# Performance work log

Hardware: AMD Instinct MI355X
Metric: run time of the kernel (lower is better)

The kernel has to match this reference:

```python
import jax, jax.numpy as jnp
import numpy as np

HEADS = 8
DIM_HEAD = 64
SCALE = DIM_HEAD ** -0.5


def setup_inputs() -> dict:
    key = jax.random.key(0)
    k1, k2, k3 = jax.random.split(key, 3)
    b, n, dim = 2, 4096, 512
    inner = HEADS * DIM_HEAD
    x = jax.random.normal(k1, (b, n, dim), dtype=jnp.float32)
    w_qkv = jax.random.normal(k2, (dim, 3 * inner), dtype=jnp.float32) * (dim ** -0.5)
    w_out = jax.random.normal(k3, (inner, dim), dtype=jnp.float32) * (inner ** -0.5)
    b_out = jnp.zeros((dim,), dtype=jnp.float32)
    return {"x": x, "w_qkv": w_qkv, "w_out": w_out, "b_out": b_out}


def reference(x, w_qkv, w_out, b_out):
    b, n, dim = x.shape
    qkv = x @ w_qkv  # [b, n, 3*inner]
    q, k, v = jnp.split(qkv, 3, axis=-1)
    # b n (h d) -> b h n d
    split_heads = lambda t: t.reshape(b, n, HEADS, DIM_HEAD).transpose(0, 2, 1, 3)
    q, k, v = split_heads(q), split_heads(k), split_heads(v)
    dots = jnp.einsum('bhid,bhjd->bhij', q, k) * SCALE  # [b, h, n, n]
    attn = jax.nn.log_softmax(dots, axis=-1)  # NOTE: log-softmax, not softmax
    out = jnp.einsum('bhij,bhjd->bhid', attn, v)  # [b, h, n, d]
    out = out.transpose(0, 2, 1, 3).reshape(b, n, HEADS * DIM_HEAD)
    return out @ w_out + b_out + x
```

## Files before the change

kernel.cpp:

```cpp
#include <hip/hip_runtime.h>
#include <stdint.h>

#define NSEQ   4096
#define BATCH  2
#define NHEAD  8
#define DHEAD  64
#define DIM    512
#define NQKV   1536
#define MROWS  (BATCH*NSEQ)
#define NBH    (BATCH*NHEAD)

typedef float  f32x4 __attribute__((ext_vector_type(4)));
typedef short  s16x8 __attribute__((ext_vector_type(8)));

__device__ __forceinline__ unsigned short f2b(float f){
  unsigned int u = __float_as_uint(f);
  u += 0x7FFFu + ((u >> 16) & 1u);
  return (unsigned short)(u >> 16);
}
__device__ __forceinline__ float b2f(unsigned short h){
  return __uint_as_float(((unsigned int)h) << 16);
}
__device__ __forceinline__ void gld_lds16(const void* g, void* l){
  __builtin_amdgcn_global_load_lds((const __attribute__((address_space(1))) unsigned int*)g,
                                   (__attribute__((address_space(3))) unsigned int*)l, 16, 0, 0);
}

__global__ void k_cvt(const float* __restrict__ in, unsigned short* __restrict__ out, int n4){
  int i = blockIdx.x*blockDim.x + threadIdx.x;
  if (i < n4){
    float4 v = ((const float4*)in)[i];
    ushort4 o;
    o.x = f2b(v.x); o.y = f2b(v.y); o.z = f2b(v.z); o.w = f2b(v.w);
    ((ushort4*)out)[i] = o;
  }
}

__global__ void k_transpose(const float* __restrict__ in, unsigned short* __restrict__ out, int R, int C){
  __shared__ float t[32][33];
  const int cb = blockIdx.x*32, rb = blockIdx.y*32;
  const int tx = threadIdx.x & 31, ty = threadIdx.x >> 5;
  #pragma unroll
  for (int s = 0; s < 32; s += 8) t[ty+s][tx] = in[(size_t)(rb+ty+s)*C + cb + tx];
  __syncthreads();
  #pragma unroll
  for (int s = 0; s < 32; s += 8) out[(size_t)(cb+ty+s)*R + rb + tx] = f2b(t[tx][ty+s]);
}

__global__ __launch_bounds__(256) void k_qkv_gemm(
    const unsigned short* __restrict__ A,
    const unsigned short* __restrict__ Bt,
    unsigned short* __restrict__ qbuf, unsigned short* __restrict__ kbuf,
    unsigned short* __restrict__ vbuf){
  __shared__ __align__(16) unsigned short at[128*32];
  __shared__ __align__(16) unsigned short bt[128*32];
  const int n0 = blockIdx.x*128, m0 = blockIdx.y*128;
  const int tid = threadIdx.x, w = tid>>6, lane = tid&63;
  const int wr = (w>>1)*64, wc = (w&1)*64;
  f32x4 acc[4][4] = {};
  for (int ks = 0; ks < 16; ++ks){
    const int k0 = ks*32;
    #pragma unroll
    for (int i = 0; i < 2; ++i){
      const int slot = w*2 + i;
      const int r = slot*16 + (lane>>2);
      const int ch = (lane&3) ^ (r&3);
      gld_lds16(A  + (size_t)(m0+r)*DIM + k0 + ch*8, (char*)at + slot*1024);
      gld_lds16(Bt + (size_t)(n0+r)*DIM + k0 + ch*8, (char*)bt + slot*1024);
    }
    __syncthreads();
    s16x8 af[4], bfr[4];
    #pragma unroll
    for (int f = 0; f < 4; ++f){
      const int rr = wr + f*16 + (lane&15);
      af[f]  = *(const s16x8*)((const char*)at + rr*64 + ((((lane>>4)) ^ (rr&3))<<4));
      const int cc = wc + f*16 + (lane&15);
      bfr[f] = *(const s16x8*)((const char*)bt + cc*64 + ((((lane>>4)) ^ (cc&3))<<4));
    }
    #pragma unroll
    for (int fr = 0; fr < 4; ++fr)
      #pragma unroll
      for (int fc = 0; fc < 4; ++fc)
        acc[fr][fc] = __builtin_amdgcn_mfma_f32_16x16x32_bf16(af[fr], bfr[fc], acc[fr][fc], 0,0,0);
    __syncthreads();
  }
  const float QS = 0.18033688011112042f;
  #pragma unroll
  for (int fr = 0; fr < 4; ++fr){
    #pragma unroll
    for (int fc = 0; fc < 4; ++fc){
      const int col = n0 + wc + fc*16 + (lane&15);
      const int which = col >> 9;
      const int h = (col & 511) >> 6;
      const int d = col & 63;
      unsigned short* dst = (which==0) ? qbuf : ((which==1) ? kbuf : vbuf);
      #pragma unroll
      for (int r = 0; r < 4; ++r){
        const int row = m0 + wr + fr*16 + (lane>>4)*4 + r;
        const int b = row >> 12, n = row & 4095;
        float v = acc[fr][fc][r];
        if (which == 0) v *= QS;
        dst[(size_t)((b*NHEAD + h)*NSEQ + n)*DHEAD + d] = f2b(v);
      }
    }
  }
}

__global__ __launch_bounds__(256) void k_tpart(
    const unsigned short* __restrict__ kbuf, const unsigned short* __restrict__ vbuf,
    unsigned short* __restrict__ tpart, float* __restrict__ vsp){
  __shared__ __align__(16) unsigned short kt[64*64];
  __shared__ __align__(16) unsigned short vt[64*64];
  const int bh = blockIdx.y, jc = blockIdx.x;
  const unsigned short* K = kbuf + (size_t)bh*NSEQ*DHEAD;
  const unsigned short* V = vbuf + (size_t)bh*NSEQ*DHEAD;
  const int tid = threadIdx.x;
  const int d1 = (tid>>4)<<2, d2 = (tid&15)<<2;
  const int j0 = jc*64;
  #pragma unroll
  for (int c = 0; c < 2; ++c){
    const int q = tid + 256*c;
    const int row = q>>3, ch = q&7;
    *(float4*)((char*)kt + row*128 + ch*16) = *(const float4*)((const char*)K + (size_t)(j0+row)*128 + ch*16);
    *(float4*)((char*)vt + row*128 + ch*16) = *(const float4*)((const char*)V + (size_t)(j0+row)*128 + ch*16);
  }
  __syncthreads();
  float accT[4][4] = {{0.f}};
  float accV[4] = {0.f,0.f,0.f,0.f};
  for (int jj = 0; jj < 64; ++jj){
    const ushort4 k4 = *(const ushort4*)(kt + jj*64 + d1);
    const ushort4 v4 = *(const ushort4*)(vt + jj*64 + d2);
    float kf[4] = {b2f(k4.x), b2f(k4.y), b2f(k4.z), b2f(k4.w)};
    float vf[4] = {b2f(v4.x), b2f(v4.y), b2f(v4.z), b2f(v4.w)};
    #pragma unroll
    for (int a = 0; a < 4; ++a)
      #pragma unroll
      for (int b = 0; b < 4; ++b) accT[a][b] += kf[a]*vf[b];
    #pragma unroll
    for (int b = 0; b < 4; ++b) accV[b] += vf[b];
  }
  unsigned short* tp = tpart + ((size_t)bh*64 + jc)*4096;
  #pragma unroll
  for (int a = 0; a < 4; ++a)
    #pragma unroll
    for (int b = 0; b < 4; ++b) tp[(d1+a)*64 + (d2+b)] = f2b(accT[a][b]);
  if (tid < 16){
    #pragma unroll
    for (int b = 0; b < 4; ++b) vsp[((size_t)bh*64 + jc)*64 + d2 + b] = accV[b];
  }
}

__global__ void k_tred(const unsigned short* __restrict__ tpart, const float* __restrict__ vsp,
                       unsigned short* __restrict__ TB, float* __restrict__ vsum){
  const int blk = blockIdx.x;
  const int bh = blk >> 4, part = blk & 15;
  const int tid = threadIdx.x;
  const int idx = part*256 + tid;
  const int dd1 = idx>>6, dd2 = idx&63;
  float s = 0.f;
  #pragma unroll 8
  for (int pr = 0; pr < 64; ++pr) s += b2f(tpart[((size_t)bh*64 + pr)*4096 + idx]);
  TB[(size_t)bh*4096 + dd2*64 + dd1] = f2b(s);
  if (part == 0 && tid < 64){
    float v = 0.f;
    #pragma unroll 8
    for (int pr = 0; pr < 64; ++pr) v += vsp[((size_t)bh*64 + pr)*64 + tid];
    vsum[bh*64 + tid] = v;
  }
}

#define ASTAGE(U, BUFI) do { \
    const int ti_ = jbase + (((U)+phase)&15); \
    const size_t o_ = (size_t)ti_*64*DHEAD; \
    char* d_ = (char*)kt[BUFI]; \
    gld_lds16(kg0 + o_, d_ + s0*1024); \
    gld_lds16(kg1 + o_, d_ + s1*1024); } while(0)

#define ATILE(BUF) do { \
    const char* buf_ = (const char*)(BUF); \
    _Pragma("unroll") \
    for (int kk = 0; kk < 4; ++kk){ \
      const int r_ = kk*16 + (lane&15); \
      const s16x8 b0_ = *(const s16x8*)(buf_ + r_*128 + ((((lane>>4))   ^ (r_&7))<<4)); \
      const s16x8 b1_ = *(const s16x8*)(buf_ + r_*128 + (((4+(lane>>4)) ^ (r_&7))<<4)); \
      f32x4 a0_ = {0.f,0.f,0.f,0.f}, a1_ = {0.f,0.f,0.f,0.f}; \
      f32x4 a2_ = {0.f,0.f,0.f,0.f}, a3_ = {0.f,0.f,0.f,0.f}; \
      __builtin_amdgcn_s_setprio(1); \
      a0_ = __builtin_amdgcn_mfma_f32_16x16x32_bf16(aq[0][0], b0_, a0_, 0,0,0); \
      a0_ = __builtin_amdgcn_mfma_f32_16x16x32_bf16(aq[0][1], b1_, a0_, 0,0,0); \
      a1_ = __builtin_amdgcn_mfma_f32_16x16x32_bf16(aq[1][0], b0_, a1_, 0,0,0); \
      a1_ = __builtin_amdgcn_mfma_f32_16x16x32_bf16(aq[1][1], b1_, a1_, 0,0,0); \
      a2_ = __builtin_amdgcn_mfma_f32_16x16x32_bf16(aq[2][0], b0_, a2_, 0,0,0); \
      a2_ = __builtin_amdgcn_mfma_f32_16x16x32_bf16(aq[2][1], b1_, a2_, 0,0,0); \
      a3_ = __builtin_amdgcn_mfma_f32_16x16x32_bf16(aq[3][0], b0_, a3_, 0,0,0); \
      a3_ = __builtin_amdgcn_mfma_f32_16x16x32_bf16(aq[3][1], b1_, a3_, 0,0,0); \
      __builtin_amdgcn_s_setprio(0); \
      _Pragma("unroll") \
      for (int rr = 0; rr < 4; ++rr){ \
        lsum[0][rr] += __builtin_amdgcn_exp2f(a0_[rr]); \
        lsum[1][rr] += __builtin_amdgcn_exp2f(a1_[rr]); \
        lsum[2][rr] += __builtin_amdgcn_exp2f(a2_[rr]); \
        lsum[3][rr] += __builtin_amdgcn_exp2f(a3_[rr]); \
      } \
    } } while(0)

#define APHASE(U, LASTW) do { \
    if (LASTW) { asm volatile("s_waitcnt vmcnt(0)" ::: "memory"); } \
    else       { asm volatile("s_waitcnt vmcnt(2)" ::: "memory"); } \
    __builtin_amdgcn_s_barrier(); \
    asm volatile("" ::: "memory"); \
    if ((U) < 14) ASTAGE((U)+2, ((U)+2)&3); \
    ATILE(kt[(U)&3]); } while(0)

__global__ __launch_bounds__(256) void k_attn(
    const unsigned short* __restrict__ qbuf, const unsigned short* __restrict__ kbuf,
    float* __restrict__ ps){
  __shared__ __align__(16) unsigned short kt[4][64*64];
  const int bid = blockIdx.x;
  const int idx = bid >> 3;
  const int bh  = ((bid & 7) << 1) + (idx >> 6);
  const int rest = idx & 63;
  const int qchunk = rest >> 2;
  const int js = rest & 3;
  const int tid = threadIdx.x, w = tid>>6, lane = tid&63;
  const int q0 = qchunk*256 + w*64;
  const unsigned short* Q = qbuf + (size_t)bh*NSEQ*DHEAD;
  const unsigned short* K = kbuf + (size_t)bh*NSEQ*DHEAD;

  s16x8 aq[4][2];
  #pragma unroll
  for (int g = 0; g < 4; ++g){
    const int qrow = q0 + g*16 + (lane&15);
    aq[g][0] = *(const s16x8*)(Q + (size_t)qrow*DHEAD + ((lane>>4)<<3));
    aq[g][1] = *(const s16x8*)(Q + (size_t)qrow*DHEAD + 32 + ((lane>>4)<<3));
  }

  const int s0 = w*2, s1 = w*2 + 1;
  const int srow0 = s0*8 + (lane>>3), srow1 = s1*8 + (lane>>3);
  const int sch = ((lane&7) ^ (lane>>3));
  const unsigned short* kg0 = K + (size_t)srow0*DHEAD + sch*8;
  const unsigned short* kg1 = K + (size_t)srow1*DHEAD + sch*8;

  const int phase = (idx*5) & 15;
  const int jbase = js*16;

  ASTAGE(0, 0);
  ASTAGE(1, 1);

  float lsum[4][4] = {};
  APHASE(0,false);  APHASE(1,false);  APHASE(2,false);  APHASE(3,false);
  APHASE(4,false);  APHASE(5,false);  APHASE(6,false);  APHASE(7,false);
  APHASE(8,false);  APHASE(9,false);  APHASE(10,false); APHASE(11,false);
  APHASE(12,false); APHASE(13,false); APHASE(14,false); APHASE(15,true);

  #pragma unroll
  for (int m = 1; m < 16; m <<= 1)
    #pragma unroll
    for (int g = 0; g < 4; ++g)
      #pragma unroll
      for (int r = 0; r < 4; ++r) lsum[g][r] += __shfl_xor(lsum[g][r], m, 16);

  if ((lane&15) == 0){
    float* pp = ps + ((size_t)js*NBH + bh)*NSEQ;
    #pragma unroll
    for (int g = 0; g < 4; ++g)
      #pragma unroll
      for (int r = 0; r < 4; ++r)
        pp[q0 + g*16 + (lane>>4)*4 + r] = lsum[g][r];
  }
}

__global__ __launch_bounds__(256) void k_attn_fin(
    const unsigned short* __restrict__ qbuf, const unsigned short* __restrict__ TB,
    const float* __restrict__ vsum, const float* __restrict__ ps,
    unsigned short* __restrict__ om){
  const int bid = blockIdx.x;
  const int bh = bid >> 6, qchunk = bid & 63;
  const int tid = threadIdx.x, w = tid>>6, lane = tid&63;
  const int q0 = qchunk*64 + w*16;
  const unsigned short* Q = qbuf + (size_t)bh*NSEQ*DHEAD;
  const int qrow = q0 + (lane&15);
  const s16x8 aq0 = *(const s16x8*)(Q + (size_t)qrow*DHEAD + ((lane>>4)<<3));
  const s16x8 aq1 = *(const s16x8*)(Q + (size_t)qrow*DHEAD + 32 + ((lane>>4)<<3));
  const float* p0 = ps + (size_t)bh*NSEQ;
  const float* p1 = ps + ((size_t)NBH   + bh)*NSEQ;
  const float* p2 = ps + ((size_t)2*NBH + bh)*NSEQ;
  const float* p3 = ps + ((size_t)3*NBH + bh)*NSEQ;
  float lse2[4];
  #pragma unroll
  for (int r = 0; r < 4; ++r){
    const int n = q0 + (lane>>4)*4 + r;
    lse2[r] = log2f((p0[n] + p1[n]) + (p2[n] + p3[n]));
  }
  const unsigned short* tb = TB + (size_t)bh*4096;
  const int b = bh>>3, h = bh&7;
  #pragma unroll
  for (int fc = 0; fc < 4; ++fc){
    const int d2 = fc*16 + (lane&15);
    const s16x8 t0 = *(const s16x8*)(tb + d2*64 + ((lane>>4)<<3));
    const s16x8 t1 = *(const s16x8*)(tb + d2*64 + 32 + ((lane>>4)<<3));
    const float vs = vsum[bh*64 + d2];
    f32x4 acc = {0.f,0.f,0.f,0.f};
    acc = __builtin_amdgcn_mfma_f32_16x16x32_bf16(aq0, t0, acc, 0,0,0);
    acc = __builtin_amdgcn_mfma_f32_16x16x32_bf16(aq1, t1, acc, 0,0,0);
    #pragma unroll
    for (int r = 0; r < 4; ++r){
      const int n = q0 + (lane>>4)*4 + r;
      const float val = 0.6931471805599453f * (acc[r] - lse2[r]*vs);
      om[((size_t)b*NSEQ + n)*DIM + h*DHEAD + d2] = f2b(val);
    }
  }
}

__global__ __launch_bounds__(256) void k_out_gemm(
    const unsigned short* __restrict__ A,
    const unsigned short* __restrict__ Bt,
    const float* __restrict__ bias, const float* __restrict__ xres,
    float* __restrict__ out){
  __shared__ __align__(16) unsigned short at[128*32];
  __shared__ __align__(16) unsigned short bt[128*32];
  const int n0 = blockIdx.x*128, m0 = blockIdx.y*128;
  const int tid = threadIdx.x, w = tid>>6, lane = tid&63;
  const int wr = (w>>1)*64, wc = (w&1)*64;
  f32x4 acc[4][4] = {};
  for (int ks = 0; ks < 16; ++ks){
    const int k0 = ks*32;
    #pragma unroll
    for (int i = 0; i < 2; ++i){
      const int slot = w*2 + i;
      const int r = slot*16 + (lane>>2);
      const int ch = (lane&3) ^ (r&3);
      gld_lds16(A  + (size_t)(m0+r)*DIM + k0 + ch*8, (char*)at + slot*1024);
      gld_lds16(Bt + (size_t)(n0+r)*DIM + k0 + ch*8, (char*)bt + slot*1024);
    }
    __syncthreads();
    s16x8 af[4], bfr[4];
    #pragma unroll
    for (int f = 0; f < 4; ++f){
      const int rr = wr + f*16 + (lane&15);
      af[f]  = *(const s16x8*)((const char*)at + rr*64 + ((((lane>>4)) ^ (rr&3))<<4));
      const int cc = wc + f*16 + (lane&15);
      bfr[f] = *(const s16x8*)((const char*)bt + cc*64 + ((((lane>>4)) ^ (cc&3))<<4));
    }
    #pragma unroll
    for (int fr = 0; fr < 4; ++fr)
      #pragma unroll
      for (int fc = 0; fc < 4; ++fc)
        acc[fr][fc] = __builtin_amdgcn_mfma_f32_16x16x32_bf16(af[fr], bfr[fc], acc[fr][fc], 0,0,0);
    __syncthreads();
  }
  #pragma unroll
  for (int fr = 0; fr < 4; ++fr){
    #pragma unroll
    for (int fc = 0; fc < 4; ++fc){
      const int col = n0 + wc + fc*16 + (lane&15);
      const float bb = bias[col];
      #pragma unroll
      for (int r = 0; r < 4; ++r){
        const int row = m0 + wr + fr*16 + (lane>>4)*4 + r;
        out[(size_t)row*DIM + col] = acc[fr][fc][r] + bb + xres[(size_t)row*DIM + col];
      }
    }
  }
}

extern "C" void kernel_launch(void* const* d_in, const int* in_sizes, int n_in,
                              void* d_out, int out_size, void* d_ws, size_t ws_size,
                              hipStream_t stream){
  const float* x    = (const float*)d_in[0];
  const float* wqkv = (const float*)d_in[1];
  const float* wout = (const float*)d_in[2];
  const float* bout = (const float*)d_in[3];
  float* out = (float*)d_out;

  char* p = (char*)d_ws;
  unsigned short* xb   = (unsigned short*)p; p += (size_t)MROWS*DIM*2;
  unsigned short* wqT  = (unsigned short*)p; p += (size_t)NQKV*DIM*2;
  unsigned short* woT  = (unsigned short*)p; p += (size_t)DIM*DIM*2;
  unsigned short* qbuf = (unsigned short*)p; p += (size_t)NBH*NSEQ*DHEAD*2;
  unsigned short* kbuf = (unsigned short*)p; p += (size_t)NBH*NSEQ*DHEAD*2;
  unsigned short* vbuf = (unsigned short*)p; p += (size_t)NBH*NSEQ*DHEAD*2;
  unsigned short* tpart= (unsigned short*)p; p += (size_t)NBH*64*4096*2;
  float* vsp           = (float*)p;          p += (size_t)NBH*64*64*4;
  unsigned short* TB   = (unsigned short*)p; p += (size_t)NBH*64*64*2;
  float* vsum          = (float*)p;          p += (size_t)NBH*64*4;
  unsigned short* om   = (unsigned short*)p; p += (size_t)MROWS*DIM*2;
  float* ps            = (float*)p;          p += (size_t)4*NBH*NSEQ*4;

  k_cvt<<<dim3((MROWS*DIM/4 + 255)/256), dim3(256), 0, stream>>>(x, xb, MROWS*DIM/4);
  k_transpose<<<dim3(NQKV/32, DIM/32), dim3(256), 0, stream>>>(wqkv, wqT, DIM, NQKV);
  k_transpose<<<dim3(DIM/32, DIM/32), dim3(256), 0, stream>>>(wout, woT, DIM, DIM);
  k_qkv_gemm<<<dim3(NQKV/128, MROWS/128), dim3(256), 0, stream>>>(xb, wqT, qbuf, kbuf, vbuf);
  k_tpart<<<dim3(64, NBH), dim3(256), 0, stream>>>(kbuf, vbuf, tpart, vsp);
  k_tred<<<dim3(256), dim3(256), 0, stream>>>(tpart, vsp, TB, vsum);
  k_attn<<<dim3(1024), dim3(256), 0, stream>>>(qbuf, kbuf, ps);
  k_attn_fin<<<dim3(1024), dim3(256), 0, stream>>>(qbuf, TB, vsum, ps, om);
  k_out_gemm<<<dim3(DIM/128, MROWS/128), dim3(256), 0, stream>>>(om, woT, bout, x, out);
}
```

Baseline: 127.3 us.

## Give each attention wave private K ring buffer and merge prep kernels

The attention kernel now has each wave stream its own 16-row K slices into a private LDS ring, with no block-wide barriers. All four waves share the same 64 query rows but cover different key slices, and the grid grows from 1024 to 4096 blocks. The per-row exp-sums are written to 16 partial slots instead of 4, and the finalize kernel reduces all 16. The bf16 convert and two weight transposes are merged into one launch. This removes barrier stalls and two kernel launches, at the cost of more partial-sum traffic and four times as many blocks, each reloading Q.

```diff
diff --git a/kernel.cpp b/kernel.cpp
--- a/kernel.cpp
+++ b/kernel.cpp
@@ -26,25 +26,33 @@
                                    (__attribute__((address_space(3))) unsigned int*)l, 16, 0, 0);
 }
 
-__global__ void k_cvt(const float* __restrict__ in, unsigned short* __restrict__ out, int n4){
-  int i = blockIdx.x*blockDim.x + threadIdx.x;
-  if (i < n4){
-    float4 v = ((const float4*)in)[i];
+__global__ void k_prep(const float* __restrict__ x, unsigned short* __restrict__ xb,
+                       const float* __restrict__ wqkv, unsigned short* __restrict__ wqT,
+                       const float* __restrict__ wout, unsigned short* __restrict__ woT){
+  __shared__ float t[32][33];
+  const int b = blockIdx.x;
+  if (b < 4096){
+    const int i = b*256 + threadIdx.x;
+    float4 v = ((const float4*)x)[i];
     ushort4 o;
     o.x = f2b(v.x); o.y = f2b(v.y); o.z = f2b(v.z); o.w = f2b(v.w);
-    ((ushort4*)out)[i] = o;
-  }
-}
-
-__global__ void k_transpose(const float* __restrict__ in, unsigned short* __restrict__ out, int R, int C){
-  __shared__ float t[32][33];
-  const int cb = blockIdx.x*32, rb = blockIdx.y*32;
-  const int tx = threadIdx.x & 31, ty = threadIdx.x >> 5;
-  #pragma unroll
-  for (int s = 0; s < 32; s += 8) t[ty+s][tx] = in[(size_t)(rb+ty+s)*C + cb + tx];
-  __syncthreads();
-  #pragma unroll
-  for (int s = 0; s < 32; s += 8) out[(size_t)(cb+ty+s)*R + rb + tx] = f2b(t[tx][ty+s]);
+    ((ushort4*)xb)[i] = o;
+  } else {
+    const float* in; unsigned short* out; int R, C, cb, rb;
+    if (b < 4096 + 768){
+      const int q = b - 4096; in = wqkv; out = wqT; R = DIM; C = NQKV;
+      cb = (q % 48)*32; rb = (q / 48)*32;
+    } else {
+      const int q = b - 4096 - 768; in = wout; out = woT; R = DIM; C = DIM;
+      cb = (q & 15)*32; rb = (q >> 4)*32;
+    }
+    const int tx = threadIdx.x & 31, ty = threadIdx.x >> 5;
+    #pragma unroll
+    for (int s = 0; s < 32; s += 8) t[ty+s][tx] = in[(size_t)(rb+ty+s)*C + cb + tx];
+    __syncthreads();
+    #pragma unroll
+    for (int s = 0; s < 32; s += 8) out[(size_t)(cb+ty+s)*R + rb + tx] = f2b(t[tx][ty+s]);
+  }
 }
 
 __global__ __launch_bounds__(256) void k_qkv_gemm(
@@ -169,61 +177,50 @@
   }
 }
 
-#define ASTAGE(U, BUFI) do { \
-    const int ti_ = jbase + (((U)+phase)&15); \
-    const size_t o_ = (size_t)ti_*64*DHEAD; \
-    char* d_ = (char*)kt[BUFI]; \
-    gld_lds16(kg0 + o_, d_ + s0*1024); \
-    gld_lds16(kg1 + o_, d_ + s1*1024); } while(0)
-
-#define ATILE(BUF) do { \
-    const char* buf_ = (const char*)(BUF); \
+#define ASTG(SIDX, RING) do { \
+    const size_t go_ = (size_t)((SIDX)*4 + w)*16*DHEAD; \
+    char* d_ = ldsw + (RING)*2048; \
+    gld_lds16(kg0 + go_, d_); \
+    gld_lds16(kg1 + go_, d_ + 1024); } while(0)
+
+#define ACOMP(S) do { \
+    const char* bp_ = ldsw + ((S)&3)*2048; \
+    const s16x8 b0_ = *(const s16x8*)(bp_ + off0); \
+    const s16x8 b1_ = *(const s16x8*)(bp_ + off1); \
+    f32x4 a0_ = {0.f,0.f,0.f,0.f}, a1_ = {0.f,0.f,0.f,0.f}; \
+    f32x4 a2_ = {0.f,0.f,0.f,0.f}, a3_ = {0.f,0.f,0.f,0.f}; \
+    __builtin_amdgcn_s_setprio(1); \
+    a0_ = __builtin_amdgcn_mfma_f32_16x16x32_bf16(aq[0][0], b0_, a0_, 0,0,0); \
+    a0_ = __builtin_amdgcn_mfma_f32_16x16x32_bf16(aq[0][1], b1_, a0_, 0,0,0); \
+    a1_ = __builtin_amdgcn_mfma_f32_16x16x32_bf16(aq[1][0], b0_, a1_, 0,0,0); \
+    a1_ = __builtin_amdgcn_mfma_f32_16x16x32_bf16(aq[1][1], b1_, a1_, 0,0,0); \
+    a2_ = __builtin_amdgcn_mfma_f32_16x16x32_bf16(aq[2][0], b0_, a2_, 0,0,0); \
+    a2_ = __builtin_amdgcn_mfma_f32_16x16x32_bf16(aq[2][1], b1_, a2_, 0,0,0); \
+    a3_ = __builtin_amdgcn_mfma_f32_16x16x32_bf16(aq[3][0], b0_, a3_, 0,0,0); \
+    a3_ = __builtin_amdgcn_mfma_f32_16x16x32_bf16(aq[3][1], b1_, a3_, 0,0,0); \
+    __builtin_amdgcn_s_setprio(0); \
     _Pragma("unroll") \
-    for (int kk = 0; kk < 4; ++kk){ \
-      const int r_ = kk*16 + (lane&15); \
-      const s16x8 b0_ = *(const s16x8*)(buf_ + r_*128 + ((((lane>>4))   ^ (r_&7))<<4)); \
-      const s16x8 b1_ = *(const s16x8*)(buf_ + r_*128 + (((4+(lane>>4)) ^ (r_&7))<<4)); \
-      f32x4 a0_ = {0.f,0.f,0.f,0.f}, a1_ = {0.f,0.f,0.f,0.f}; \
-      f32x4 a2_ = {0.f,0.f,0.f,0.f}, a3_ = {0.f,0.f,0.f,0.f}; \
-      __builtin_amdgcn_s_setprio(1); \
-      a0_ = __builtin_amdgcn_mfma_f32_16x16x32_bf16(aq[0][0], b0_, a0_, 0,0,0); \
-      a0_ = __builtin_amdgcn_mfma_f32_16x16x32_bf16(aq[0][1], b1_, a0_, 0,0,0); \
-      a1_ = __builtin_amdgcn_mfma_f32_16x16x32_bf16(aq[1][0], b0_, a1_, 0,0,0); \
-      a1_ = __builtin_amdgcn_mfma_f32_16x16x32_bf16(aq[1][1], b1_, a1_, 0,0,0); \
-      a2_ = __builtin_amdgcn_mfma_f32_16x16x32_bf16(aq[2][0], b0_, a2_, 0,0,0); \
-      a2_ = __builtin_amdgcn_mfma_f32_16x16x32_bf16(aq[2][1], b1_, a2_, 0,0,0); \
-      a3_ = __builtin_amdgcn_mfma_f32_16x16x32_bf16(aq[3][0], b0_, a3_, 0,0,0); \
-      a3_ = __builtin_amdgcn_mfma_f32_16x16x32_bf16(aq[3][1], b1_, a3_, 0,0,0); \
-      __builtin_amdgcn_s_setprio(0); \
-      _Pragma("unroll") \
-      for (int rr = 0; rr < 4; ++rr){ \
-        lsum[0][rr] += __builtin_amdgcn_exp2f(a0_[rr]); \
-        lsum[1][rr] += __builtin_amdgcn_exp2f(a1_[rr]); \
-        lsum[2][rr] += __builtin_amdgcn_exp2f(a2_[rr]); \
-        lsum[3][rr] += __builtin_amdgcn_exp2f(a3_[rr]); \
-      } \
+    for (int rr = 0; rr < 4; ++rr){ \
+      lsum[0][rr] += __builtin_amdgcn_exp2f(a0_[rr]); \
+      lsum[1][rr] += __builtin_amdgcn_exp2f(a1_[rr]); \
+      lsum[2][rr] += __builtin_amdgcn_exp2f(a2_[rr]); \
+      lsum[3][rr] += __builtin_amdgcn_exp2f(a3_[rr]); \
     } } while(0)
 
-#define APHASE(U, LASTW) do { \
-    if (LASTW) { asm volatile("s_waitcnt vmcnt(0)" ::: "memory"); } \
-    else       { asm volatile("s_waitcnt vmcnt(2)" ::: "memory"); } \
-    __builtin_amdgcn_s_barrier(); \
-    asm volatile("" ::: "memory"); \
-    if ((U) < 14) ASTAGE((U)+2, ((U)+2)&3); \
-    ATILE(kt[(U)&3]); } while(0)
+#define VMW(N) asm volatile("s_waitcnt vmcnt(" #N ")" ::: "memory")
 
 __global__ __launch_bounds__(256) void k_attn(
     const unsigned short* __restrict__ qbuf, const unsigned short* __restrict__ kbuf,
     float* __restrict__ ps){
-  __shared__ __align__(16) unsigned short kt[4][64*64];
+  __shared__ __align__(16) char kt[4*8192];
   const int bid = blockIdx.x;
   const int idx = bid >> 3;
-  const int bh  = ((bid & 7) << 1) + (idx >> 6);
-  const int rest = idx & 63;
-  const int qchunk = rest >> 2;
+  const int bh  = ((bid & 7) << 1) + (idx >> 8);
+  const int rest = idx & 255;
+  const int qc = rest >> 2;
   const int js = rest & 3;
   const int tid = threadIdx.x, w = tid>>6, lane = tid&63;
-  const int q0 = qchunk*256 + w*64;
+  const int q0 = qc*64;
   const unsigned short* Q = qbuf + (size_t)bh*NSEQ*DHEAD;
   const unsigned short* K = kbuf + (size_t)bh*NSEQ*DHEAD;
 
@@ -235,23 +232,34 @@
     aq[g][1] = *(const s16x8*)(Q + (size_t)qrow*DHEAD + 32 + ((lane>>4)<<3));
   }
 
-  const int s0 = w*2, s1 = w*2 + 1;
-  const int srow0 = s0*8 + (lane>>3), srow1 = s1*8 + (lane>>3);
+  char* ldsw = kt + w*8192;
   const int sch = ((lane&7) ^ (lane>>3));
-  const unsigned short* kg0 = K + (size_t)srow0*DHEAD + sch*8;
-  const unsigned short* kg1 = K + (size_t)srow1*DHEAD + sch*8;
-
-  const int phase = (idx*5) & 15;
-  const int jbase = js*16;
-
-  ASTAGE(0, 0);
-  ASTAGE(1, 1);
+  const unsigned short* kg0 = K + (size_t)(js*1024 + (lane>>3))*DHEAD + sch*8;
+  const unsigned short* kg1 = kg0 + (size_t)8*DHEAD;
+
+  const int r_ = lane&15, hi = lane>>4;
+  const int off0 = r_*128 + (((hi)   ^ (r_&7))<<4);
+  const int off1 = r_*128 + (((4+hi) ^ (r_&7))<<4);
+
+  ASTG(0,0); ASTG(1,1); ASTG(2,2);
 
   float lsum[4][4] = {};
-  APHASE(0,false);  APHASE(1,false);  APHASE(2,false);  APHASE(3,false);
-  APHASE(4,false);  APHASE(5,false);  APHASE(6,false);  APHASE(7,false);
-  APHASE(8,false);  APHASE(9,false);  APHASE(10,false); APHASE(11,false);
-  APHASE(12,false); APHASE(13,false); APHASE(14,false); APHASE(15,true);
+  ASTG(3,3);  VMW(6); ACOMP(0);
+  ASTG(4,0);  VMW(6); ACOMP(1);
+  ASTG(5,1);  VMW(6); ACOMP(2);
+  ASTG(6,2);  VMW(6); ACOMP(3);
+  ASTG(7,3);  VMW(6); ACOMP(4);
+  ASTG(8,0);  VMW(6); ACOMP(5);
+  ASTG(9,1);  VMW(6); ACOMP(6);
+  ASTG(10,2); VMW(6); ACOMP(7);
+  ASTG(11,3); VMW(6); ACOMP(8);
+  ASTG(12,0); VMW(6); ACOMP(9);
+  ASTG(13,1); VMW(6); ACOMP(10);
+  ASTG(14,2); VMW(6); ACOMP(11);
+  ASTG(15,3); VMW(6); ACOMP(12);
+              VMW(4); ACOMP(13);
+              VMW(2); ACOMP(14);
+              VMW(0); ACOMP(15);
 
   #pragma unroll
   for (int m = 1; m < 16; m <<= 1)
@@ -261,7 +269,7 @@
       for (int r = 0; r < 4; ++r) lsum[g][r] += __shfl_xor(lsum[g][r], m, 16);
 
   if ((lane&15) == 0){
-    float* pp = ps + ((size_t)js*NBH + bh)*NSEQ;
+    float* pp = ps + ((size_t)(js*4 + w)*NBH + bh)*NSEQ;
     #pragma unroll
     for (int g = 0; g < 4; ++g)
       #pragma unroll
@@ -282,15 +290,16 @@
   const int qrow = q0 + (lane&15);
   const s16x8 aq0 = *(const s16x8*)(Q + (size_t)qrow*DHEAD + ((lane>>4)<<3));
   const s16x8 aq1 = *(const s16x8*)(Q + (size_t)qrow*DHEAD + 32 + ((lane>>4)<<3));
-  const float* p0 = ps + (size_t)bh*NSEQ;
-  const float* p1 = ps + ((size_t)NBH   + bh)*NSEQ;
-  const float* p2 = ps + ((size_t)2*NBH + bh)*NSEQ;
-  const float* p3 = ps + ((size_t)3*NBH + bh)*NSEQ;
+  const float* pb = ps + (size_t)bh*NSEQ;
   float lse2[4];
   #pragma unroll
   for (int r = 0; r < 4; ++r){
     const int n = q0 + (lane>>4)*4 + r;
-    lse2[r] = log2f((p0[n] + p1[n]) + (p2[n] + p3[n]));
+    float s = 0.f;
+    #pragma unroll
+    for (int slot = 0; slot < 16; ++slot)
+      s += pb[(size_t)slot*NBH*NSEQ + n];
+    lse2[r] = log2f(s);
   }
   const unsigned short* tb = TB + (size_t)bh*4096;
   const int b = bh>>3, h = bh&7;
@@ -385,15 +394,13 @@
   unsigned short* TB   = (unsigned short*)p; p += (size_t)NBH*64*64*2;
   float* vsum          = (float*)p;          p += (size_t)NBH*64*4;
   unsigned short* om   = (unsigned short*)p; p += (size_t)MROWS*DIM*2;
-  float* ps            = (float*)p;          p += (size_t)4*NBH*NSEQ*4;
-
-  k_cvt<<<dim3((MROWS*DIM/4 + 255)/256), dim3(256), 0, stream>>>(x, xb, MROWS*DIM/4);
-  k_transpose<<<dim3(NQKV/32, DIM/32), dim3(256), 0, stream>>>(wqkv, wqT, DIM, NQKV);
-  k_transpose<<<dim3(DIM/32, DIM/32), dim3(256), 0, stream>>>(wout, woT, DIM, DIM);
+  float* ps            = (float*)p;          p += (size_t)16*NBH*NSEQ*4;
+
+  k_prep<<<dim3(4096 + 768 + 256), dim3(256), 0, stream>>>(x, xb, wqkv, wqT, wout, woT);
   k_qkv_gemm<<<dim3(NQKV/128, MROWS/128), dim3(256), 0, stream>>>(xb, wqT, qbuf, kbuf, vbuf);
   k_tpart<<<dim3(64, NBH), dim3(256), 0, stream>>>(kbuf, vbuf, tpart, vsp);
   k_tred<<<dim3(256), dim3(256), 0, stream>>>(tpart, vsp, TB, vsum);
-  k_attn<<<dim3(1024), dim3(256), 0, stream>>>(qbuf, kbuf, ps);
+  k_attn<<<dim3(4096), dim3(256), 0, stream>>>(qbuf, kbuf, ps);
   k_attn_fin<<<dim3(1024), dim3(256), 0, stream>>>(qbuf, TB, vsum, ps, om);
   k_out_gemm<<<dim3(DIM/128, MROWS/128), dim3(256), 0, stream>>>(om, woT, bout, x, out);
 }
```

New measurement: 136.5 us. 7.2% more time.
